# Optimization experiments

Measured on AMD Instinct MI355X. Metric: run time of the kernel, lower is better.

The kernel has to match this reference:

```python
import jax, jax.numpy as jnp
import numpy as np

B, S, F, H = 2, 2048, 1024, 16
HD = F // H  # head_dim = 64


def rope_embedding(length: int, features: int) -> jnp.ndarray:
    # Faithful copy of the module's unusual RoPE: emb = concat[sin, cos] used as an
    # elementwise multiplier, with symmetric averaging for positions > 0.
    base = 10000.0
    inv_freq = 1.0 / base ** (jnp.arange(0, features, 2, dtype=jnp.float32) / features)
    sinusoid = jnp.einsum('i,j->ij', jnp.arange(length, dtype=jnp.float32), inv_freq)
    sin = jnp.sin(sinusoid)
    cos = jnp.cos(sinusoid)  # features even, so no trailing-column drop
    emb = jnp.concatenate([sin, cos], axis=1)[:, None, :]  # [L, 1, HD]
    if length > 1:
        emb_sym = (emb[1:] + emb[1:][::-1]) / 2.0
        emb = jnp.concatenate([emb[:1], emb_sym], axis=0)
    return emb


def setup_inputs() -> dict:
    key = jax.random.key(0)
    ks = jax.random.split(key, 6)
    scale = 1.0 / np.sqrt(F)
    kv = jax.random.normal(ks[0], (B, S, F), dtype=jnp.float32)
    q = jax.random.normal(ks[1], (B, S, F), dtype=jnp.float32)
    Wq = jax.random.normal(ks[2], (F, F), dtype=jnp.float32) * scale
    Wk = jax.random.normal(ks[3], (F, F), dtype=jnp.float32) * scale
    Wv = jax.random.normal(ks[4], (F, F), dtype=jnp.float32) * scale
    Wo = jax.random.normal(ks[5], (F, F), dtype=jnp.float32) * scale
    mask = jnp.tril(jnp.ones((S, S), dtype=bool))[None, None]  # causal [1,1,S,S]
    return {"kv": kv, "q": q, "Wq": Wq, "Wk": Wk, "Wv": Wv, "Wo": Wo, "mask": mask}


def reference(kv, q, Wq, Wk, Wv, Wo, mask):
    # Dense projections (use_bias=False)
    query = (q @ Wq).reshape(B, S, H, HD)
    key_ = (kv @ Wk).reshape(B, S, H, HD)
    value = (kv @ Wv).reshape(B, S, H, HD)
    # Inline RoPE multiply (module's variant)
    emb = rope_embedding(S, HD)  # [S, 1, HD]
    query = query * emb
    key_ = key_ * emb
    # Scores [B, H, Sq, Sk], scale, mask, softmax
    aw = jnp.einsum('bqhd,bkhd->bhqk', query, key_) / jnp.sqrt(jnp.float32(HD))
    aw = jnp.where(mask, aw, jnp.finfo(jnp.float32).min)
    aw = jax.nn.softmax(aw, axis=-1)
    out = jnp.einsum('bhqk,bkhd->bqhd', aw, value).reshape(B, S, F)
    return out @ Wo
```

## Files before the change

kernel.cpp:

```cpp
#include <hip/hip_runtime.h>

typedef unsigned short u16;
typedef unsigned int u32;

#define S_LEN 2048
#define FEAT 1024
#define NHEAD 16
#define HDIM 64
#define NBATCH 2
#define NROWS (NBATCH * S_LEN)

typedef float f32x4 __attribute__((ext_vector_type(4)));
typedef short s16x8 __attribute__((ext_vector_type(8)));
typedef u32 u32x2 __attribute__((ext_vector_type(2)));

#define LOG2E 1.4426950408889634f

__device__ inline u16 f2bf(float f) {
  u32 u = __float_as_uint(f);
  return (u16)((u + 0x7fffu + ((u >> 16) & 1u)) >> 16);
}

__device__ inline u32 cvt_pk_bf16(float lo, float hi) {
  u32 r;
  asm("v_cvt_pk_bf16_f32 %0, %1, %2" : "=v"(r) : "v"(lo), "v"(hi));
  return r;
}

__device__ inline float fexp2(float x) { return __builtin_amdgcn_exp2f(x); }

__device__ inline f32x4 mfma16(s16x8 a, s16x8 b, f32x4 c) {
  return __builtin_amdgcn_mfma_f32_16x16x32_bf16(a, b, c, 0, 0, 0);
}

typedef __attribute__((address_space(1))) void gvoid;
typedef __attribute__((address_space(3))) void lvoid;
__device__ inline void gload_lds16(const void* g, void* l) {
  __builtin_amdgcn_global_load_lds((gvoid*)g, (lvoid*)l, 16, 0, 0);
}

__device__ inline int swz64(int p) { return p ^ (((p >> 7) & 7) << 4); }

struct us4 { u16 x, y, z, w; };
__global__ __launch_bounds__(256) void prep_kernel(
    const float* __restrict__ q, const float* __restrict__ kv,
    const float* __restrict__ Wq, const float* __restrict__ Wk,
    const float* __restrict__ Wv, const float* __restrict__ Wo,
    u16* __restrict__ qbf, u16* __restrict__ kvbf,
    u16* __restrict__ WqT, u16* __restrict__ WkT,
    u16* __restrict__ WvT, u16* __restrict__ WoT,
    float* __restrict__ emb) {
  __shared__ float tile[32][33];
  int bid = blockIdx.x, tid = threadIdx.x;
  const int n4each = NROWS * FEAT / 4;
  if (bid < 8192) {
    int i = bid * 256 + tid;
    const float* in = q;
    u16* out = qbf;
    if (i >= n4each) { i -= n4each; in = kv; out = kvbf; }
    float4 v = ((const float4*)in)[i];
    us4 o;
    o.x = f2bf(v.x); o.y = f2bf(v.y); o.z = f2bf(v.z); o.w = f2bf(v.w);
    ((us4*)out)[i] = o;
  } else if (bid < 12288) {
    int idx = bid - 8192;
    int z = idx >> 10, rem = idx & 1023;
    int by = rem >> 5, bx = rem & 31;
    const float* W = z == 0 ? Wq : z == 1 ? Wk : z == 2 ? Wv : Wo;
    u16* O = z == 0 ? WqT : z == 1 ? WkT : z == 2 ? WvT : WoT;
    int tx = tid & 31, ty = tid >> 5;
    int bi = bx * 32, bo = by * 32;
#pragma unroll
    for (int r = 0; r < 32; r += 8) tile[ty + r][tx] = W[(bi + ty + r) * FEAT + bo + tx];
    __syncthreads();
#pragma unroll
    for (int r = 0; r < 32; r += 8) O[(bo + ty + r) * FEAT + bi + tx] = f2bf(tile[tx][ty + r]);
  } else {
    int i = (bid - 12288) * 256 + tid;
    if (i >= S_LEN * HDIM) return;
    int p = i >> 6, d = i & 63, j = d & 31;
    float invf = exp2f(-13.287712379549449f * (float)j / 32.0f);
    float a1 = (float)p * invf;
    float v1 = (d < 32) ? sinf(a1) : cosf(a1);
    float e;
    if (p == 0) {
      e = v1;
    } else {
      float a2 = (float)(S_LEN - p) * invf;
      float v2 = (d < 32) ? sinf(a2) : cosf(a2);
      e = 0.5f * (v1 + v2);
    }
    emb[i] = e;
  }
}

__global__ __launch_bounds__(256, 3) void gemm_qkv(
    const u16* __restrict__ qbf, const u16* __restrict__ kvbf,
    const u16* __restrict__ WqT, const u16* __restrict__ WkT, const u16* __restrict__ WvT,
    u16* __restrict__ Qb, u16* __restrict__ Kx, u16* __restrict__ Vx,
    const float* __restrict__ emb) {
  __shared__ __align__(16) u16 lA[3][128 * 32];
  __shared__ __align__(16) u16 lB[3][128 * 32];
  const int K = FEAT;
  int t = threadIdx.x;
  int w = t >> 6, l = t & 63;
  int lr = l & 15, lk = l >> 4;
  int flat = blockIdx.y * 32 + blockIdx.x;
  int xcd = flat & 7, idx = flat >> 3;
  int cx = xcd & 3, cy = xcd >> 2;
  int bx = cx * 8 + (idx & 7);
  int yy = cy * 12 + (idx >> 3);
  int mode = yy >> 3;
  int row0 = bx * 128, col0 = (yy & 7) * 128;
  int wm = w >> 1, wn = w & 1;

  const u16* A = mode == 0 ? qbf : kvbf;
  const u16* Bt = mode == 0 ? WqT : mode == 1 ? WkT : WvT;
  u16* Out = mode == 0 ? Qb : mode == 1 ? Kx : Vx;

  f32x4 acc[4][4] = {};

  int P0 = t * 16, P1 = P0 + 4096;
  int L0 = swz64(P0), L1 = swz64(P1);
  const char* Ab = (const char*)A;
  const char* Bb = (const char*)Bt;
  size_t aOff0 = (size_t)(row0 + (L0 >> 6)) * (K * 2) + (L0 & 63);
  size_t aOff1 = (size_t)(row0 + (L1 >> 6)) * (K * 2) + (L1 & 63);
  size_t bOff0 = (size_t)(col0 + (L0 >> 6)) * (K * 2) + (L0 & 63);
  size_t bOff1 = (size_t)(col0 + (L1 >> 6)) * (K * 2) + (L1 & 63);

  auto stage = [&](int buf, int kt) {
    int kb = kt * 64;
    gload_lds16(Ab + aOff0 + kb, (char*)&lA[buf][0] + w * 1024);
    gload_lds16(Ab + aOff1 + kb, (char*)&lA[buf][0] + w * 1024 + 4096);
    gload_lds16(Bb + bOff0 + kb, (char*)&lB[buf][0] + w * 1024);
    gload_lds16(Bb + bOff1 + kb, (char*)&lB[buf][0] + w * 1024 + 4096);
  };

  stage(0, 0);
  const int NK = K / 32;
  int bufc = 0;
  for (int kt = 0; kt < NK; ++kt) {
    int nb3 = (bufc == 2) ? 0 : bufc + 1;
    if (kt + 1 < NK) {
      stage(nb3, kt + 1);
      asm volatile("s_waitcnt vmcnt(4)" ::: "memory");
    } else {
      asm volatile("s_waitcnt vmcnt(0)" ::: "memory");
    }
    __builtin_amdgcn_s_barrier();

    const char* la = (const char*)&lA[bufc][0];
    const char* lb = (const char*)&lB[bufc][0];
    s16x8 af[4], bfr[4];
#pragma unroll
    for (int mi = 0; mi < 4; ++mi) {
      int byte = (wm * 64 + mi * 16 + lr) * 64 + lk * 16;
      af[mi] = *(const s16x8*)(la + swz64(byte));
    }
#pragma unroll
    for (int ni = 0; ni < 4; ++ni) {
      int byte = (wn * 64 + ni * 16 + lr) * 64 + lk * 16;
      bfr[ni] = *(const s16x8*)(lb + swz64(byte));
    }
    __builtin_amdgcn_s_setprio(1);
#pragma unroll
    for (int mi = 0; mi < 4; ++mi)
#pragma unroll
      for (int ni = 0; ni < 4; ++ni)
        acc[mi][ni] = mfma16(af[mi], bfr[ni], acc[mi][ni]);
    __builtin_amdgcn_s_setprio(0);
    bufc = nb3;
  }

  int rb = row0 + wm * 64 + lk * 4;
  int cb = col0 + wn * 64 + lr;
#pragma unroll
  for (int mi = 0; mi < 4; ++mi)
#pragma unroll
    for (int ni = 0; ni < 4; ++ni) {
      int col = cb + ni * 16;
      int h = col >> 6, d = col & (HDIM - 1);
      if (mode <= 1) {
#pragma unroll
        for (int r = 0; r < 4; ++r) {
          int row = rb + mi * 16 + r;
          int b = row >> 11, s = row & (S_LEN - 1);
          float v = acc[mi][ni][r] * emb[s * HDIM + d];
          if (mode == 0) v *= 0.125f;
          Out[(((b << 4) + h) * S_LEN + s) * HDIM + d] = f2bf(v);
        }
      } else {
        int s0 = rb + mi * 16;
        int b = s0 >> 11, s = s0 & (S_LEN - 1);
        us4 o;
        o.x = f2bf(acc[mi][ni][0]); o.y = f2bf(acc[mi][ni][1]);
        o.z = f2bf(acc[mi][ni][2]); o.w = f2bf(acc[mi][ni][3]);
        *(us4*)&Out[(((b << 4) + h) * HDIM + d) * S_LEN + s] = o;
      }
    }
}

__global__ __launch_bounds__(256, 2) void gemm_oproj(
    const u16* __restrict__ A, const u16* __restrict__ Bt, float* __restrict__ Out) {
  __shared__ __align__(16) u16 lA[3][128 * 32];
  __shared__ __align__(16) u16 lB[3][64 * 32];
  const int K = FEAT, N = FEAT;
  int t = threadIdx.x;
  int w = t >> 6, l = t & 63;
  int lr = l & 15, lk = l >> 4;
  int flat = blockIdx.y * 32 + blockIdx.x;
  int xcd = flat & 7, idx = flat >> 3;
  int cx = xcd & 3, cy = xcd >> 2;
  int bx = cx * 8 + (idx & 7);
  int by = cy * 8 + (idx >> 3);
  int row0 = bx * 128, col0 = by * 64;
  int wm = w >> 1, wn = w & 1;

  f32x4 acc[4][2] = {};

  int P0 = t * 16, P1 = P0 + 4096;
  int L0 = swz64(P0), L1 = swz64(P1);
  const char* Ab = (const char*)A;
  const char* Bb = (const char*)Bt;
  size_t aOff0 = (size_t)(row0 + (L0 >> 6)) * (K * 2) + (L0 & 63);
  size_t aOff1 = (size_t)(row0 + (L1 >> 6)) * (K * 2) + (L1 & 63);
  size_t bOff0 = (size_t)(col0 + (L0 >> 6)) * (K * 2) + (L0 & 63);

  auto stage = [&](int buf, int kt) {
    int kb = kt * 64;
    gload_lds16(Ab + aOff0 + kb, (char*)&lA[buf][0] + w * 1024);
    gload_lds16(Ab + aOff1 + kb, (char*)&lA[buf][0] + w * 1024 + 4096);
    gload_lds16(Bb + bOff0 + kb, (char*)&lB[buf][0] + w * 1024);
  };

  stage(0, 0);
  const int NK = K / 32;
  int bufc = 0;
  for (int kt = 0; kt < NK; ++kt) {
    int nb3 = (bufc == 2) ? 0 : bufc + 1;
    if (kt + 1 < NK) {
      stage(nb3, kt + 1);
      asm volatile("s_waitcnt vmcnt(3)" ::: "memory");
    } else {
      asm volatile("s_waitcnt vmcnt(0)" ::: "memory");
    }
    __builtin_amdgcn_s_barrier();

    const char* la = (const char*)&lA[bufc][0];
    const char* lb = (const char*)&lB[bufc][0];
    s16x8 af[4], bfr[2];
#pragma unroll
    for (int mi = 0; mi < 4; ++mi) {
      int byte = (wm * 64 + mi * 16 + lr) * 64 + lk * 16;
      af[mi] = *(const s16x8*)(la + swz64(byte));
    }
#pragma unroll
    for (int ni = 0; ni < 2; ++ni) {
      int byte = (wn * 32 + ni * 16 + lr) * 64 + lk * 16;
      bfr[ni] = *(const s16x8*)(lb + swz64(byte));
    }
    __builtin_amdgcn_s_setprio(1);
#pragma unroll
    for (int mi = 0; mi < 4; ++mi)
#pragma unroll
      for (int ni = 0; ni < 2; ++ni)
        acc[mi][ni] = mfma16(af[mi], bfr[ni], acc[mi][ni]);
    __builtin_amdgcn_s_setprio(0);
    bufc = nb3;
  }

  int rb = row0 + wm * 64 + lk * 4;
  int cb = col0 + wn * 32 + lr;
#pragma unroll
  for (int mi = 0; mi < 4; ++mi)
#pragma unroll
    for (int ni = 0; ni < 2; ++ni)
#pragma unroll
      for (int r = 0; r < 4; ++r)
        Out[(rb + mi * 16 + r) * N + cb + ni * 16] = acc[mi][ni][r];
}

__global__ __launch_bounds__(256, 4) void attn_kernel(
    const u16* __restrict__ Q, const u16* __restrict__ Kb,
    const u16* __restrict__ Vt, u16* __restrict__ AO) {
  __shared__ __align__(16) u16 lK[2][64 * 64];
  __shared__ __align__(16) u16 lV[2][64 * 64];
  __shared__ __align__(16) u16 lP[4][16 * 64];

  int t = threadIdx.x, w = t >> 6, l = t & 63;
  int lr = l & 15, lk = l >> 4;
  int bid = blockIdx.x;
  int xcd = bid & 7, r = bid >> 3;
  int bh = xcd * 4 + (r & 3);
  int s = r >> 2;
  int qt = (s < 8) ? 2 * s
         : (s < 16) ? 2 * (s - 8) + 1
         : (s < 24) ? 31 - 2 * (s - 16)
         : 30 - 2 * (s - 24);
  int nt = qt + 1;
  const u16* Qp = Q + bh * (S_LEN * HDIM);
  const char* Kc = (const char*)(Kb + bh * (S_LEN * HDIM));
  const char* Vc = (const char*)(Vt + bh * (HDIM * S_LEN));
  int b = bh >> 4, h = bh & 15;
  int sw = (lr & 7) << 4;

  int P0 = w * 1024 + l * 16;
  int row0 = P0 >> 7;
  int srcK0 = P0 ^ ((row0 & 7) << 4);
  int srcV0 = row0 * 4096 + ((P0 & 127) ^ ((row0 & 7) << 4));

  auto stage = [&](int buf, int kt) {
    gload_lds16(Kc + kt * 8192 + srcK0,          (char*)&lK[buf][0] + w * 1024);
    gload_lds16(Kc + kt * 8192 + srcK0 + 4096,   (char*)&lK[buf][0] + w * 1024 + 4096);
    gload_lds16(Vc + kt * 128 + srcV0,           (char*)&lV[buf][0] + w * 1024);
    gload_lds16(Vc + kt * 128 + srcV0 + 131072,  (char*)&lV[buf][0] + w * 1024 + 4096);
  };

  int qrow = qt * 64 + w * 16 + lr;
  s16x8 q0 = *(const s16x8*)&Qp[qrow * HDIM + lk * 8];
  s16x8 q1 = *(const s16x8*)&Qp[qrow * HDIM + lk * 8 + 32];

  f32x4 oacc[4] = {};
  float ls = 0.f;
  char* plb = (char*)&lP[w][0];

  stage(0, 0);
  asm volatile("s_waitcnt vmcnt(0)" ::: "memory");
  __builtin_amdgcn_s_barrier();
  int buf = 0;
  for (int g = 0; g < nt; ++g) {
    if (g + 1 < nt) stage(buf ^ 1, g + 1);
    const char* kb = (const char*)&lK[buf][0];
    const char* vb = (const char*)&lV[buf][0];

    s16x8 vf[4][2];
#pragma unroll
    for (int nd = 0; nd < 4; ++nd)
#pragma unroll
      for (int ks = 0; ks < 2; ++ks)
        vf[nd][ks] = *(const s16x8*)(vb + nd * 2048 + lr * 128 + ((lk * 16 + ks * 64) ^ sw));

    f32x4 s4[4] = {};
    __builtin_amdgcn_s_setprio(1);
#pragma unroll
    for (int nb = 0; nb < 4; ++nb)
#pragma unroll
      for (int ks = 0; ks < 2; ++ks) {
        s16x8 kf = *(const s16x8*)(kb + nb * 2048 + lr * 128 + ((lk * 16 + ks * 64) ^ sw));
        s4[nb] = mfma16(kf, ks ? q1 : q0, s4[nb]);
      }
    __builtin_amdgcn_s_setprio(0);

    if (g == nt - 1) {
#pragma unroll
      for (int nb = 0; nb < 4; ++nb)
#pragma unroll
        for (int rr = 0; rr < 4; ++rr)
          if (g * 64 + nb * 16 + lk * 4 + rr > qrow) s4[nb][rr] = -3.0e38f;
    }

    float rs = 0.f;
    float p[4][4];
#pragma unroll
    for (int nb = 0; nb < 4; ++nb)
#pragma unroll
      for (int rr = 0; rr < 4; ++rr) {
        float pv = fexp2((s4[nb][rr] - 8.0f) * LOG2E);
        p[nb][rr] = pv;
        rs += pv;
      }
    ls += rs;
#pragma unroll
    for (int nb = 0; nb < 4; ++nb) {
      u32x2 pw;
      pw.x = cvt_pk_bf16(p[nb][0], p[nb][1]);
      pw.y = cvt_pk_bf16(p[nb][2], p[nb][3]);
      int off = (lr * 128 + nb * 32 + lk * 8) ^ sw;
      *(u32x2*)(plb + off) = pw;
    }
    asm volatile("s_waitcnt lgkmcnt(0)" ::: "memory");
    __builtin_amdgcn_sched_barrier(0);
    s16x8 pf0 = *(const s16x8*)(plb + ((lr * 128 + lk * 16) ^ sw));
    s16x8 pf1 = *(const s16x8*)(plb + ((lr * 128 + 64 + lk * 16) ^ sw));
    __builtin_amdgcn_s_setprio(1);
#pragma unroll
    for (int nd = 0; nd < 4; ++nd) {
      oacc[nd] = mfma16(vf[nd][0], pf0, oacc[nd]);
      oacc[nd] = mfma16(vf[nd][1], pf1, oacc[nd]);
    }
    __builtin_amdgcn_s_setprio(0);

    if (g + 1 < nt) {
      asm volatile("s_waitcnt vmcnt(0)" ::: "memory");
      __builtin_amdgcn_s_barrier();
    }
    buf ^= 1;
  }

  ls += __shfl_xor(ls, 16, 64);
  ls += __shfl_xor(ls, 32, 64);
  float inv = 1.0f / ls;
  u16* dst = &AO[(b * S_LEN + qrow) * FEAT + h * HDIM + lk * 4];
#pragma unroll
  for (int nd = 0; nd < 4; ++nd) {
    us4 o;
    o.x = f2bf(oacc[nd][0] * inv);
    o.y = f2bf(oacc[nd][1] * inv);
    o.z = f2bf(oacc[nd][2] * inv);
    o.w = f2bf(oacc[nd][3] * inv);
    *(us4*)(dst + nd * 16) = o;
  }
}

extern "C" void kernel_launch(void* const* d_in, const int* in_sizes, int n_in,
                              void* d_out, int out_size, void* d_ws, size_t ws_size,
                              hipStream_t stream) {
  const float* kv = (const float*)d_in[0];
  const float* q  = (const float*)d_in[1];
  const float* Wq = (const float*)d_in[2];
  const float* Wk = (const float*)d_in[3];
  const float* Wv = (const float*)d_in[4];
  const float* Wo = (const float*)d_in[5];

  float* emb = (float*)d_ws;
  u16* qbf  = (u16*)((char*)d_ws + S_LEN * HDIM * 4);
  u16* kvbf = qbf + NROWS * FEAT;
  u16* WqT  = kvbf + NROWS * FEAT;
  u16* WkT  = WqT + FEAT * FEAT;
  u16* WvT  = WkT + FEAT * FEAT;
  u16* WoT  = WvT + FEAT * FEAT;
  u16* Qb   = WoT + FEAT * FEAT;
  u16* Kx   = Qb + NROWS * FEAT;
  u16* Vx   = Kx + NROWS * FEAT;
  u16* AO   = Vx + NROWS * FEAT;

  prep_kernel<<<12800, 256, 0, stream>>>(q, kv, Wq, Wk, Wv, Wo,
                                         qbf, kvbf, WqT, WkT, WvT, WoT, emb);

  gemm_qkv<<<dim3(NROWS / 128, 24), 256, 0, stream>>>(qbf, kvbf, WqT, WkT, WvT,
                                                      Qb, Kx, Vx, emb);

  attn_kernel<<<1024, 256, 0, stream>>>(Qb, Kx, Vx, AO);

  gemm_oproj<<<dim3(NROWS / 128, FEAT / 64), 256, 0, stream>>>(AO, WoT, (float*)d_out);
}
```

Measured before the change: 105.9 us.

## Fuse fp32-to-bf16 activation conversion into QKV GEMM A-tile loading

Removes the separate pass that converts q and kv to bf16 in the prep kernel. The QKV GEMM now reads fp32 activations straight into registers, converts them with packed bf16 conversion, and writes them to LDS. The pipeline is restructured to prefetch two stages ahead. This avoids writing and re-reading the bf16 copies of the activations, but each GEMM block now reads twice as many A bytes from global memory and spends VALU and register work on conversion inside the main loop.

```diff
diff --git a/kernel.cpp b/kernel.cpp
--- a/kernel.cpp
+++ b/kernel.cpp
@@ -13,6 +13,7 @@
 typedef float f32x4 __attribute__((ext_vector_type(4)));
 typedef short s16x8 __attribute__((ext_vector_type(8)));
 typedef u32 u32x2 __attribute__((ext_vector_type(2)));
+typedef u32 u32x4 __attribute__((ext_vector_type(4)));
 
 #define LOG2E 1.4426950408889634f
 
@@ -43,28 +44,15 @@
 
 struct us4 { u16 x, y, z, w; };
 __global__ __launch_bounds__(256) void prep_kernel(
-    const float* __restrict__ q, const float* __restrict__ kv,
     const float* __restrict__ Wq, const float* __restrict__ Wk,
     const float* __restrict__ Wv, const float* __restrict__ Wo,
-    u16* __restrict__ qbf, u16* __restrict__ kvbf,
     u16* __restrict__ WqT, u16* __restrict__ WkT,
     u16* __restrict__ WvT, u16* __restrict__ WoT,
     float* __restrict__ emb) {
   __shared__ float tile[32][33];
   int bid = blockIdx.x, tid = threadIdx.x;
-  const int n4each = NROWS * FEAT / 4;
-  if (bid < 8192) {
-    int i = bid * 256 + tid;
-    const float* in = q;
-    u16* out = qbf;
-    if (i >= n4each) { i -= n4each; in = kv; out = kvbf; }
-    float4 v = ((const float4*)in)[i];
-    us4 o;
-    o.x = f2bf(v.x); o.y = f2bf(v.y); o.z = f2bf(v.z); o.w = f2bf(v.w);
-    ((us4*)out)[i] = o;
-  } else if (bid < 12288) {
-    int idx = bid - 8192;
-    int z = idx >> 10, rem = idx & 1023;
+  if (bid < 4096) {
+    int z = bid >> 10, rem = bid & 1023;
     int by = rem >> 5, bx = rem & 31;
     const float* W = z == 0 ? Wq : z == 1 ? Wk : z == 2 ? Wv : Wo;
     u16* O = z == 0 ? WqT : z == 1 ? WkT : z == 2 ? WvT : WoT;
@@ -76,7 +64,7 @@
 #pragma unroll
     for (int r = 0; r < 32; r += 8) O[(bo + ty + r) * FEAT + bi + tx] = f2bf(tile[tx][ty + r]);
   } else {
-    int i = (bid - 12288) * 256 + tid;
+    int i = (bid - 4096) * 256 + tid;
     if (i >= S_LEN * HDIM) return;
     int p = i >> 6, d = i & 63, j = d & 31;
     float invf = exp2f(-13.287712379549449f * (float)j / 32.0f);
@@ -95,7 +83,7 @@
 }
 
 __global__ __launch_bounds__(256, 3) void gemm_qkv(
-    const u16* __restrict__ qbf, const u16* __restrict__ kvbf,
+    const float* __restrict__ qf, const float* __restrict__ kvf,
     const u16* __restrict__ WqT, const u16* __restrict__ WkT, const u16* __restrict__ WvT,
     u16* __restrict__ Qb, u16* __restrict__ Kx, u16* __restrict__ Vx,
     const float* __restrict__ emb) {
@@ -114,42 +102,59 @@
   int row0 = bx * 128, col0 = (yy & 7) * 128;
   int wm = w >> 1, wn = w & 1;
 
-  const u16* A = mode == 0 ? qbf : kvbf;
+  const float* Af = mode == 0 ? qf : kvf;
   const u16* Bt = mode == 0 ? WqT : mode == 1 ? WkT : WvT;
   u16* Out = mode == 0 ? Qb : mode == 1 ? Kx : Vx;
 
   f32x4 acc[4][4] = {};
 
+  int ar = t >> 2, ac = t & 3;
+  const float* aSrc0 = Af + (size_t)(row0 + ar) * K + ac * 8;
+  const float* aSrc1 = aSrc0 + (size_t)64 * K;
+  int dL0 = swz64(ar * 64 + ac * 16);
+  int dL1 = swz64(ar * 64 + ac * 16 + 4096);
+
   int P0 = t * 16, P1 = P0 + 4096;
   int L0 = swz64(P0), L1 = swz64(P1);
-  const char* Ab = (const char*)A;
   const char* Bb = (const char*)Bt;
-  size_t aOff0 = (size_t)(row0 + (L0 >> 6)) * (K * 2) + (L0 & 63);
-  size_t aOff1 = (size_t)(row0 + (L1 >> 6)) * (K * 2) + (L1 & 63);
   size_t bOff0 = (size_t)(col0 + (L0 >> 6)) * (K * 2) + (L0 & 63);
   size_t bOff1 = (size_t)(col0 + (L1 >> 6)) * (K * 2) + (L1 & 63);
 
-  auto stage = [&](int buf, int kt) {
+  float4 avn[4];
+  auto loadA = [&](int kt) {
+    const float* s0 = aSrc0 + kt * 32;
+    const float* s1 = aSrc1 + kt * 32;
+    avn[0] = *(const float4*)s0; avn[1] = *(const float4*)(s0 + 4);
+    avn[2] = *(const float4*)s1; avn[3] = *(const float4*)(s1 + 4);
+  };
+  auto writeA = [&](int buf) {
+    u32x4 d0, d1;
+    d0.x = cvt_pk_bf16(avn[0].x, avn[0].y); d0.y = cvt_pk_bf16(avn[0].z, avn[0].w);
+    d0.z = cvt_pk_bf16(avn[1].x, avn[1].y); d0.w = cvt_pk_bf16(avn[1].z, avn[1].w);
+    d1.x = cvt_pk_bf16(avn[2].x, avn[2].y); d1.y = cvt_pk_bf16(avn[2].z, avn[2].w);
+    d1.z = cvt_pk_bf16(avn[3].x, avn[3].y); d1.w = cvt_pk_bf16(avn[3].z, avn[3].w);
+    *(u32x4*)((char*)&lA[buf][0] + dL0) = d0;
+    *(u32x4*)((char*)&lA[buf][0] + dL1) = d1;
+  };
+  auto stageB = [&](int buf, int kt) {
     int kb = kt * 64;
-    gload_lds16(Ab + aOff0 + kb, (char*)&lA[buf][0] + w * 1024);
-    gload_lds16(Ab + aOff1 + kb, (char*)&lA[buf][0] + w * 1024 + 4096);
     gload_lds16(Bb + bOff0 + kb, (char*)&lB[buf][0] + w * 1024);
     gload_lds16(Bb + bOff1 + kb, (char*)&lB[buf][0] + w * 1024 + 4096);
   };
 
-  stage(0, 0);
+  loadA(0);
+  stageB(0, 0);
+  asm volatile("s_waitcnt vmcnt(2)" ::: "memory");
+  writeA(0);
+  loadA(1);
+  stageB(1, 1);
+  asm volatile("s_waitcnt vmcnt(6)" ::: "memory");
+  asm volatile("s_waitcnt lgkmcnt(0)" ::: "memory");
+  __builtin_amdgcn_s_barrier();
+
   const int NK = K / 32;
   int bufc = 0;
   for (int kt = 0; kt < NK; ++kt) {
-    int nb3 = (bufc == 2) ? 0 : bufc + 1;
-    if (kt + 1 < NK) {
-      stage(nb3, kt + 1);
-      asm volatile("s_waitcnt vmcnt(4)" ::: "memory");
-    } else {
-      asm volatile("s_waitcnt vmcnt(0)" ::: "memory");
-    }
-    __builtin_amdgcn_s_barrier();
-
     const char* la = (const char*)&lA[bufc][0];
     const char* lb = (const char*)&lB[bufc][0];
     s16x8 af[4], bfr[4];
@@ -163,6 +168,18 @@
       int byte = (wn * 64 + ni * 16 + lr) * 64 + lk * 16;
       bfr[ni] = *(const s16x8*)(lb + swz64(byte));
     }
+
+    int b1 = (bufc == 2) ? 0 : bufc + 1;
+    int b2 = (b1 == 2) ? 0 : b1 + 1;
+    if (kt + 1 < NK) {
+      asm volatile("s_waitcnt vmcnt(2)" ::: "memory");
+      writeA(b1);
+      if (kt + 2 < NK) {
+        loadA(kt + 2);
+        stageB(b2, kt + 2);
+      }
+    }
+
     __builtin_amdgcn_s_setprio(1);
 #pragma unroll
     for (int mi = 0; mi < 4; ++mi)
@@ -170,7 +187,17 @@
       for (int ni = 0; ni < 4; ++ni)
         acc[mi][ni] = mfma16(af[mi], bfr[ni], acc[mi][ni]);
     __builtin_amdgcn_s_setprio(0);
-    bufc = nb3;
+
+    if (kt + 1 < NK) {
+      if (kt + 2 < NK) {
+        asm volatile("s_waitcnt vmcnt(6)" ::: "memory");
+      } else {
+        asm volatile("s_waitcnt vmcnt(0)" ::: "memory");
+      }
+      asm volatile("s_waitcnt lgkmcnt(0)" ::: "memory");
+      __builtin_amdgcn_s_barrier();
+    }
+    bufc = b1;
   }
 
   int rb = row0 + wm * 64 + lk * 4;
@@ -424,9 +451,7 @@
   const float* Wo = (const float*)d_in[5];
 
   float* emb = (float*)d_ws;
-  u16* qbf  = (u16*)((char*)d_ws + S_LEN * HDIM * 4);
-  u16* kvbf = qbf + NROWS * FEAT;
-  u16* WqT  = kvbf + NROWS * FEAT;
+  u16* WqT  = (u16*)((char*)d_ws + S_LEN * HDIM * 4);
   u16* WkT  = WqT + FEAT * FEAT;
   u16* WvT  = WkT + FEAT * FEAT;
   u16* WoT  = WvT + FEAT * FEAT;
@@ -435,10 +460,9 @@
   u16* Vx   = Kx + NROWS * FEAT;
   u16* AO   = Vx + NROWS * FEAT;
 
-  prep_kernel<<<12800, 256, 0, stream>>>(q, kv, Wq, Wk, Wv, Wo,
-                                         qbf, kvbf, WqT, WkT, WvT, WoT, emb);
-
-  gemm_qkv<<<dim3(NROWS / 128, 24), 256, 0, stream>>>(qbf, kvbf, WqT, WkT, WvT,
+  prep_kernel<<<4608, 256, 0, stream>>>(Wq, Wk, Wv, Wo, WqT, WkT, WvT, WoT, emb);
+
+  gemm_qkv<<<dim3(NROWS / 128, 24), 256, 0, stream>>>(q, kv, WqT, WkT, WvT,
                                                       Qb, Kx, Vx, emb);
 
   attn_kernel<<<1024, 256, 0, stream>>>(Qb, Kx, Vx, AO);
```

Result: faster. 103.4 us (-2.4%).
